# Kernel optimization log

Measured on AMD Instinct MI355X. Metric: run time of the kernel, lower is better.

Reference implementation:

```python
import jax, jax.numpy as jnp
import numpy as np
from math import floor

B, ST, C, H, W = 4, 9, 3, 288, 288
K = 5           # kernel_size
DH, DW = 3, 3   # stride (ang_y, ang_x)
OH, OW = 96, 96 # output_size


def setup_inputs() -> dict:
    key = jax.random.key(0)
    k1, k2, k3 = jax.random.split(key, 3)
    lf = jax.random.uniform(k1, (B, ST, C, H, W), dtype=jnp.float32)
    # learned position-varying kernels: (st_out, st_in, 1, oh, ow, k*k)
    weights = jax.random.normal(k2, (ST, ST, 1, OH, OW, K * K), dtype=jnp.float32) * 0.02
    biases = jax.random.normal(k3, (ST, OH, OW), dtype=jnp.float32) * 0.01
    return {"lf": lf, "weights": weights, "biases": biases}


def reference(lf, weights, biases):
    b, st, c, h, w = lf.shape
    # padding identical to the torch module (F.pad order: left,right,top,bottom)
    pad_x = (OW - 1) * DW + (K - w)
    pad_y = (OH - 1) * DH + (K - h)
    pl = floor(K / 2); pr = pad_x - pl
    pt = floor(K / 2); pb = pad_y - pt
    lfp = jnp.pad(lf, ((0, 0), (0, 0), (0, 0), (pt, pb), (pl, pr)))
    # unfold(3,K,DH).unfold(4,K,DW) then flatten (kh,kw) -> k2 with kh slow, kw fast
    # patches: (b, st_in, c, oh, ow, K*K)
    patches = jnp.stack(
        [lfp[..., i:i + (OH - 1) * DH + 1:DH, j:j + (OW - 1) * DW + 1:DW]
         for i in range(K) for j in range(K)], axis=-1)
    # per-position contraction over (st_in, k2); avoids the torch broadcast blowup
    out = jnp.einsum('bichwk,oihwk->bochw', patches, weights[:, :, 0])
    out = out + biases[None, :, None]  # (1, st_out, 1, oh, ow)
    return jnp.clip(out, 0.0, 1.0)
```

## Files before the change

### kernel.cpp

```cpp
#include <hip/hip_runtime.h>

#define NPIX 9216
#define PLANE 82944
#define WPL 230400

typedef float f4v __attribute__((ext_vector_type(4)));

__global__ __launch_bounds__(128)
void lfk20(const float* __restrict__ lf, const float* __restrict__ wts,
           const float* __restrict__ bias, float* __restrict__ out)
{
    __shared__ float ldsW[2][1344];

    const int tid  = threadIdx.x;
    const int wv   = tid >> 6;
    const int lane = tid & 63;
    const int px   = lane & 15;
    const int b    = lane >> 4;
    const int bid  = blockIdx.x;
    const int swz  = (bid & 7) * 216 + (bid >> 3);
    const int tile = swz / 3;
    const int og   = swz - tile * 3;
    const int oh   = tile / 6;
    const int tc   = tile - oh * 6;
    const int g    = tile * 16 + px;
    const int ow   = tc * 16 + px;
    const int y0   = oh * 3 - 2;
    const int x0   = ow * 3 - 2;
    const int xcl  = (x0 < 0) ? 0 : x0;
    const bool xneg = (x0 < 0);
    const bool tc0  = (tc == 0);
    const bool oh0  = (oh == 0);

    float* const myl = &ldsW[wv][0];
    const int i0 = wv ? 5 : 0;
    const int i1 = wv ? 9 : 5;

    const bool srow = (lane < 48);
    const int soc = lane >> 4;
    const int spx = lane & 15;
    const long swbase = (long)((og * 3 + soc) * 9) * WPL + tile * 400 + spx * 25;
    float* const swdst = myl + soc * 448 + spx * 28;

    f4v r0, r1, r2, r3, r4, r5; float r6;
    auto stageLoad = [&](int i) {
        if (srow) {
            const float* gp = wts + swbase + (long)i * WPL;
            __builtin_memcpy(&r0, gp,      16);
            __builtin_memcpy(&r1, gp + 4,  16);
            __builtin_memcpy(&r2, gp + 8,  16);
            __builtin_memcpy(&r3, gp + 12, 16);
            __builtin_memcpy(&r4, gp + 16, 16);
            __builtin_memcpy(&r5, gp + 20, 16);
            r6 = gp[24];
        }
    };
    auto scatterWrite = [&]() {
        if (srow) {
            *(f4v*)(swdst +  0) = r0;
            *(f4v*)(swdst +  4) = r1;
            *(f4v*)(swdst +  8) = r2;
            *(f4v*)(swdst + 12) = r3;
            *(f4v*)(swdst + 16) = r4;
            *(f4v*)(swdst + 20) = r5;
            swdst[24] = r6;
        }
    };

    auto loadP = [&](f4v (&A)[5], float (&E)[5], int i, int c) {
        const float* rb = lf + ((b * 9 + i) * 3 + c) * PLANE + xcl;
        #pragma unroll
        for (int kh = 0; kh < 5; ++kh) {
            const int y = y0 + kh;
            if (!oh0 || y >= 0) {
                const float* rp = rb + y * 288;
                __builtin_memcpy(&A[kh], rp, 16);
                E[kh] = rp[4];
            } else { A[kh] = (f4v)0.f; E[kh] = 0.f; }
        }
    };

    float wk[3][25];
    float acc[3][3] = {{0,0,0},{0,0,0},{0,0,0}};

    auto doFMA = [&](const f4v (&A)[5], const float (&E)[5], int c) {
        #pragma unroll
        for (int kh = 0; kh < 5; ++kh) {
            const f4v a = A[kh]; const float e = E[kh];
            float q0,q1,q2,q3,q4;
            if (tc0) {
                q0 = xneg ? 0.f : a.x;  q1 = xneg ? 0.f : a.y;
                q2 = xneg ? a.x : a.z;  q3 = xneg ? a.y : a.w;
                q4 = xneg ? a.z : e;
            } else { q0=a.x; q1=a.y; q2=a.z; q3=a.w; q4=e; }
            #pragma unroll
            for (int oc = 0; oc < 3; ++oc) {
                acc[oc][c] = fmaf(wk[oc][kh*5+0], q0, acc[oc][c]);
                acc[oc][c] = fmaf(wk[oc][kh*5+1], q1, acc[oc][c]);
                acc[oc][c] = fmaf(wk[oc][kh*5+2], q2, acc[oc][c]);
                acc[oc][c] = fmaf(wk[oc][kh*5+3], q3, acc[oc][c]);
                acc[oc][c] = fmaf(wk[oc][kh*5+4], q4, acc[oc][c]);
            }
        }
    };

    f4v PA[5], PB[5]; float EA[5], EB[5];

    stageLoad(i0);
    scatterWrite();
    loadP(PA, EA, i0, 0);

    #pragma unroll 1
    for (int i = i0; i < i1; ++i) {
        const bool more = (i < i1 - 1);

        #pragma unroll
        for (int oc = 0; oc < 3; ++oc) {
            const float* wr = myl + oc * 448 + px * 28;
            const f4v* wq = (const f4v*)wr;
            const f4v u0=wq[0], u1=wq[1], u2=wq[2], u3=wq[3], u4=wq[4], u5=wq[5];
            wk[oc][0]=u0.x;  wk[oc][1]=u0.y;  wk[oc][2]=u0.z;  wk[oc][3]=u0.w;
            wk[oc][4]=u1.x;  wk[oc][5]=u1.y;  wk[oc][6]=u1.z;  wk[oc][7]=u1.w;
            wk[oc][8]=u2.x;  wk[oc][9]=u2.y;  wk[oc][10]=u2.z; wk[oc][11]=u2.w;
            wk[oc][12]=u3.x; wk[oc][13]=u3.y; wk[oc][14]=u3.z; wk[oc][15]=u3.w;
            wk[oc][16]=u4.x; wk[oc][17]=u4.y; wk[oc][18]=u4.z; wk[oc][19]=u4.w;
            wk[oc][20]=u5.x; wk[oc][21]=u5.y; wk[oc][22]=u5.z; wk[oc][23]=u5.w;
            wk[oc][24]=wr[24];
        }

        if (more) stageLoad(i + 1);

        loadP(PB, EB, i, 1);
        doFMA(PA, EA, 0);
        loadP(PA, EA, i, 2);
        doFMA(PB, EB, 1);
        doFMA(PA, EA, 2);

        if (more) {
            scatterWrite();
            loadP(PA, EA, i + 1, 0);
        }
    }

    if (wv != 0) {
        #pragma unroll
        for (int oc = 0; oc < 3; ++oc)
            #pragma unroll
            for (int c = 0; c < 3; ++c)
                myl[lane * 9 + oc * 3 + c] = acc[oc][c];
    }
    __syncthreads();

    if (wv == 0) {
        #pragma unroll
        for (int oc = 0; oc < 3; ++oc)
            #pragma unroll
            for (int c = 0; c < 3; ++c)
                acc[oc][c] += ldsW[1][lane * 9 + oc * 3 + c];
        #pragma unroll
        for (int oc = 0; oc < 3; ++oc) {
            const int o = og * 3 + oc;
            const float bo = bias[o * NPIX + g];
            #pragma unroll
            for (int c = 0; c < 3; ++c) {
                float v = acc[oc][c] + bo;
                v = fminf(fmaxf(v, 0.f), 1.f);
                out[((b * 9 + o) * 3 + c) * NPIX + g] = v;
            }
        }
    }
}

extern "C" void kernel_launch(void* const* d_in, const int* in_sizes, int n_in,
                              void* d_out, int out_size, void* d_ws, size_t ws_size,
                              hipStream_t stream) {
    const float* lf   = (const float*)d_in[0];
    const float* wts  = (const float*)d_in[1];
    const float* bias = (const float*)d_in[2];
    float* out = (float*)d_out;
    (void)d_ws; (void)ws_size; (void)in_sizes; (void)n_in; (void)out_size;

    dim3 grid(576 * 3);
    dim3 block(128);
    lfk20<<<grid, block, 0, stream>>>(lf, wts, bias, out);
}
```

Before: 32.62 us.

## Split input-view reduction across blocks with atomic accumulation and epilogue kernel

Each block now handles a single input view instead of a wave pair covering all nine, which raises the block count ninefold and uses one-wave blocks. Partial sums go to global memory through atomicAdd after a memset, and a second kernel adds the bias and clamps. This removes the serial per-block loop over views and the LDS cross-wave reduction. In exchange it adds a memset and an extra kernel launch, nine-way atomic contention per output, a second pass over the output, and floating-point sums whose order is no longer fixed.

```diff
diff --git a/kernel.cpp b/kernel.cpp
--- a/kernel.cpp
+++ b/kernel.cpp
@@ -3,24 +3,26 @@
 #define NPIX 9216
 #define PLANE 82944
 #define WPL 230400
+#define NOUT 995328
 
 typedef float f4v __attribute__((ext_vector_type(4)));
 
-__global__ __launch_bounds__(128)
-void lfk20(const float* __restrict__ lf, const float* __restrict__ wts,
-           const float* __restrict__ bias, float* __restrict__ out)
+__global__ __launch_bounds__(64)
+void lfp1(const float* __restrict__ lf, const float* __restrict__ wts,
+          float* __restrict__ out)
 {
-    __shared__ float ldsW[2][1344];
+    __shared__ float ldsW[1344];
 
-    const int tid  = threadIdx.x;
-    const int wv   = tid >> 6;
-    const int lane = tid & 63;
+    const int lane = threadIdx.x;
     const int px   = lane & 15;
     const int b    = lane >> 4;
     const int bid  = blockIdx.x;
-    const int swz  = (bid & 7) * 216 + (bid >> 3);
-    const int tile = swz / 3;
-    const int og   = swz - tile * 3;
+    const int swz  = (bid & 7) * 1944 + (bid >> 3);
+    const int tile = swz / 27;
+    const int rem  = swz - tile * 27;
+    const int og   = rem / 9;
+    const int ii   = rem - og * 9;
+
     const int oh   = tile / 6;
     const int tc   = tile - oh * 6;
     const int g    = tile * 16 + px;
@@ -32,43 +34,33 @@
     const bool tc0  = (tc == 0);
     const bool oh0  = (oh == 0);
 
-    float* const myl = &ldsW[wv][0];
-    const int i0 = wv ? 5 : 0;
-    const int i1 = wv ? 9 : 5;
-
     const bool srow = (lane < 48);
     const int soc = lane >> 4;
     const int spx = lane & 15;
-    const long swbase = (long)((og * 3 + soc) * 9) * WPL + tile * 400 + spx * 25;
-    float* const swdst = myl + soc * 448 + spx * 28;
+    const long swbase = (long)((og * 3 + soc) * 9 + ii) * WPL + tile * 400 + spx * 25;
+    float* const swdst = ldsW + soc * 448 + spx * 28;
 
-    f4v r0, r1, r2, r3, r4, r5; float r6;
-    auto stageLoad = [&](int i) {
-        if (srow) {
-            const float* gp = wts + swbase + (long)i * WPL;
-            __builtin_memcpy(&r0, gp,      16);
-            __builtin_memcpy(&r1, gp + 4,  16);
-            __builtin_memcpy(&r2, gp + 8,  16);
-            __builtin_memcpy(&r3, gp + 12, 16);
-            __builtin_memcpy(&r4, gp + 16, 16);
-            __builtin_memcpy(&r5, gp + 20, 16);
-            r6 = gp[24];
-        }
-    };
-    auto scatterWrite = [&]() {
-        if (srow) {
-            *(f4v*)(swdst +  0) = r0;
-            *(f4v*)(swdst +  4) = r1;
-            *(f4v*)(swdst +  8) = r2;
-            *(f4v*)(swdst + 12) = r3;
-            *(f4v*)(swdst + 16) = r4;
-            *(f4v*)(swdst + 20) = r5;
-            swdst[24] = r6;
-        }
-    };
+    if (srow) {
+        const float* gp = wts + swbase;
+        f4v r0, r1, r2, r3, r4, r5; float r6;
+        __builtin_memcpy(&r0, gp,      16);
+        __builtin_memcpy(&r1, gp + 4,  16);
+        __builtin_memcpy(&r2, gp + 8,  16);
+        __builtin_memcpy(&r3, gp + 12, 16);
+        __builtin_memcpy(&r4, gp + 16, 16);
+        __builtin_memcpy(&r5, gp + 20, 16);
+        r6 = gp[24];
+        *(f4v*)(swdst +  0) = r0;
+        *(f4v*)(swdst +  4) = r1;
+        *(f4v*)(swdst +  8) = r2;
+        *(f4v*)(swdst + 12) = r3;
+        *(f4v*)(swdst + 16) = r4;
+        *(f4v*)(swdst + 20) = r5;
+        swdst[24] = r6;
+    }
 
-    auto loadP = [&](f4v (&A)[5], float (&E)[5], int i, int c) {
-        const float* rb = lf + ((b * 9 + i) * 3 + c) * PLANE + xcl;
+    auto loadP = [&](f4v (&A)[5], float (&E)[5], int c) {
+        const float* rb = lf + ((b * 9 + ii) * 3 + c) * PLANE + xcl;
         #pragma unroll
         for (int kh = 0; kh < 5; ++kh) {
             const int y = y0 + kh;
@@ -105,70 +97,54 @@
     };
 
     f4v PA[5], PB[5]; float EA[5], EB[5];
+    loadP(PA, EA, 0);
 
-    stageLoad(i0);
-    scatterWrite();
-    loadP(PA, EA, i0, 0);
-
-    #pragma unroll 1
-    for (int i = i0; i < i1; ++i) {
-        const bool more = (i < i1 - 1);
-
-        #pragma unroll
-        for (int oc = 0; oc < 3; ++oc) {
-            const float* wr = myl + oc * 448 + px * 28;
-            const f4v* wq = (const f4v*)wr;
-            const f4v u0=wq[0], u1=wq[1], u2=wq[2], u3=wq[3], u4=wq[4], u5=wq[5];
-            wk[oc][0]=u0.x;  wk[oc][1]=u0.y;  wk[oc][2]=u0.z;  wk[oc][3]=u0.w;
-            wk[oc][4]=u1.x;  wk[oc][5]=u1.y;  wk[oc][6]=u1.z;  wk[oc][7]=u1.w;
-            wk[oc][8]=u2.x;  wk[oc][9]=u2.y;  wk[oc][10]=u2.z; wk[oc][11]=u2.w;
-            wk[oc][12]=u3.x; wk[oc][13]=u3.y; wk[oc][14]=u3.z; wk[oc][15]=u3.w;
-            wk[oc][16]=u4.x; wk[oc][17]=u4.y; wk[oc][18]=u4.z; wk[oc][19]=u4.w;
-            wk[oc][20]=u5.x; wk[oc][21]=u5.y; wk[oc][22]=u5.z; wk[oc][23]=u5.w;
-            wk[oc][24]=wr[24];
-        }
-
-        if (more) stageLoad(i + 1);
-
-        loadP(PB, EB, i, 1);
-        doFMA(PA, EA, 0);
-        loadP(PA, EA, i, 2);
-        doFMA(PB, EB, 1);
-        doFMA(PA, EA, 2);
-
-        if (more) {
-            scatterWrite();
-            loadP(PA, EA, i + 1, 0);
-        }
+    #pragma unroll
+    for (int oc = 0; oc < 3; ++oc) {
+        const float* wr = ldsW + oc * 448 + px * 28;
+        const f4v* wq = (const f4v*)wr;
+        const f4v u0=wq[0], u1=wq[1], u2=wq[2], u3=wq[3], u4=wq[4], u5=wq[5];
+        wk[oc][0]=u0.x;  wk[oc][1]=u0.y;  wk[oc][2]=u0.z;  wk[oc][3]=u0.w;
+        wk[oc][4]=u1.x;  wk[oc][5]=u1.y;  wk[oc][6]=u1.z;  wk[oc][7]=u1.w;
+        wk[oc][8]=u2.x;  wk[oc][9]=u2.y;  wk[oc][10]=u2.z; wk[oc][11]=u2.w;
+        wk[oc][12]=u3.x; wk[oc][13]=u3.y; wk[oc][14]=u3.z; wk[oc][15]=u3.w;
+        wk[oc][16]=u4.x; wk[oc][17]=u4.y; wk[oc][18]=u4.z; wk[oc][19]=u4.w;
+        wk[oc][20]=u5.x; wk[oc][21]=u5.y; wk[oc][22]=u5.z; wk[oc][23]=u5.w;
+        wk[oc][24]=wr[24];
     }
 
-    if (wv != 0) {
+    loadP(PB, EB, 1);
+    doFMA(PA, EA, 0);
+    loadP(PA, EA, 2);
+    doFMA(PB, EB, 1);
+    doFMA(PA, EA, 2);
+
+    #pragma unroll
+    for (int oc = 0; oc < 3; ++oc) {
+        const int o = og * 3 + oc;
         #pragma unroll
-        for (int oc = 0; oc < 3; ++oc)
-            #pragma unroll
-            for (int c = 0; c < 3; ++c)
-                myl[lane * 9 + oc * 3 + c] = acc[oc][c];
+        for (int c = 0; c < 3; ++c)
+            atomicAdd(&out[((b * 9 + o) * 3 + c) * NPIX + g], acc[oc][c]);
     }
-    __syncthreads();
+}
 
-    if (wv == 0) {
-        #pragma unroll
-        for (int oc = 0; oc < 3; ++oc)
-            #pragma unroll
-            for (int c = 0; c < 3; ++c)
-                acc[oc][c] += ldsW[1][lane * 9 + oc * 3 + c];
-        #pragma unroll
-        for (int oc = 0; oc < 3; ++oc) {
-            const int o = og * 3 + oc;
-            const float bo = bias[o * NPIX + g];
-            #pragma unroll
-            for (int c = 0; c < 3; ++c) {
-                float v = acc[oc][c] + bo;
-                v = fminf(fmaxf(v, 0.f), 1.f);
-                out[((b * 9 + o) * 3 + c) * NPIX + g] = v;
-            }
-        }
+__global__ __launch_bounds__(256)
+void lfp2(float* __restrict__ out, const float* __restrict__ bias)
+{
+    const int idx4 = blockIdx.x * 256 + threadIdx.x;
+    const int f = idx4 * 4;
+    const int row = f / NPIX;
+    const int g = f - row * NPIX;
+    const int o = (row / 3) % 9;
+    f4v v, bv;
+    __builtin_memcpy(&v,  &out[f], 16);
+    __builtin_memcpy(&bv, &bias[o * NPIX + g], 16);
+    #pragma unroll
+    for (int q = 0; q < 4; ++q) {
+        float t = v[q] + bv[q];
+        v[q] = fminf(fmaxf(t, 0.f), 1.f);
     }
+    *(f4v*)&out[f] = v;
 }
 
 extern "C" void kernel_launch(void* const* d_in, const int* in_sizes, int n_in,
@@ -180,7 +156,7 @@
     float* out = (float*)d_out;
     (void)d_ws; (void)ws_size; (void)in_sizes; (void)n_in; (void)out_size;
 
-    dim3 grid(576 * 3);
-    dim3 block(128);
-    lfk20<<<grid, block, 0, stream>>>(lf, wts, bias, out);
+    hipMemsetAsync(out, 0, (size_t)NOUT * sizeof(float), stream);
+    lfp1<<<dim3(576 * 27), dim3(64), 0, stream>>>(lf, wts, out);
+    lfp2<<<dim3(972), dim3(256), 0, stream>>>(out, bias);
 }
```

Result: slower. 53.88 us (+65.2%).
